# Kernel optimization log

Measured on AMD Instinct MI355X. Metric: run time of the kernel, lower is better.

The kernel has to match this reference:

```python
import jax, jax.numpy as jnp
import numpy as np
import math

D_MODEL = 1024
N_HEADS = 16
D_K = D_MODEL // N_HEADS
B, S = 4, 2048


def setup_inputs() -> dict:
    key = jax.random.key(0)
    ks = jax.random.split(key, 11)
    std = 1.0 / math.sqrt(D_MODEL)
    inp = {
        "query": jax.random.normal(ks[0], (B, S, D_MODEL), dtype=jnp.float32),
        "key_in": jax.random.normal(ks[1], (B, S, D_MODEL), dtype=jnp.float32),
        "value": jax.random.normal(ks[2], (B, S, D_MODEL), dtype=jnp.float32),
        "Wq": jax.random.normal(ks[3], (D_MODEL, D_MODEL), dtype=jnp.float32) * std,
        "bq": jnp.zeros((D_MODEL,), dtype=jnp.float32),
        "Wk": jax.random.normal(ks[4], (D_MODEL, D_MODEL), dtype=jnp.float32) * std,
        "bk": jnp.zeros((D_MODEL,), dtype=jnp.float32),
        "Wv": jax.random.normal(ks[5], (D_MODEL, D_MODEL), dtype=jnp.float32) * std,
        "bv": jnp.zeros((D_MODEL,), dtype=jnp.float32),
        "Wo": jax.random.normal(ks[6], (D_MODEL, D_MODEL), dtype=jnp.float32) * std,
        "bo": jnp.zeros((D_MODEL,), dtype=jnp.float32),
    }
    return inp


def reference(query, key_in, value, Wq, bq, Wk, bk, Wv, bv, Wo, bo):
    b, s, _ = query.shape
    scale = math.sqrt(D_K)
    # projections: nn.Linear computes x @ W.T + b
    Q = (query @ Wq.T + bq).reshape(b, s, N_HEADS, D_K).transpose(0, 2, 1, 3)
    K = (key_in @ Wk.T + bk).reshape(b, s, N_HEADS, D_K).transpose(0, 2, 1, 3)
    V = (value @ Wv.T + bv).reshape(b, s, N_HEADS, D_K).transpose(0, 2, 1, 3)
    # [b, h, s, s]
    scores = jnp.einsum("bhqd,bhkd->bhqk", Q, K) / scale
    causal = jnp.tril(jnp.ones((s, s), dtype=bool))
    scores = jnp.where(causal[None, None, :, :], scores, jnp.float32(-1e9))
    attn = jax.nn.softmax(scores, axis=-1)
    out = jnp.einsum("bhqk,bhkd->bhqd", attn, V)
    out = out.transpose(0, 2, 1, 3).reshape(b, s, D_MODEL)
    return out @ Wo.T + bo
```

## Files before the change

kernel.cpp:

```cpp
#include <hip/hip_runtime.h>
#include <hip/hip_bf16.h>
#include <cstdint>

#define DM   1024
#define NH   16
#define DKK  64
#define BB   4
#define SS   2048

typedef __attribute__((ext_vector_type(8)))  short short8;
typedef __attribute__((ext_vector_type(4)))  float f32x4;
typedef __attribute__((ext_vector_type(16))) float f32x16;

__device__ __forceinline__ unsigned short f2bf(float f) {
    union { float f; uint32_t u; } v; v.f = f;
    uint32_t u = v.u;
    uint32_t r = (u + 0x7FFFu + ((u >> 16) & 1u)) >> 16;
    return (unsigned short)r;
}

#define GLL(src, dst) __builtin_amdgcn_global_load_lds(                      \
        (__attribute__((address_space(1))) void*)(src),                      \
        (__attribute__((address_space(3))) void*)(dst), 16, 0, 0)

__global__ void cvt_w(const float* __restrict__ wq, const float* __restrict__ wk,
                      const float* __restrict__ wv, const float* __restrict__ wo,
                      unsigned short* __restrict__ dst)
{
    int i = blockIdx.x * 256 + threadIdx.x;
    int a = i >> 17;
    int r = i & 131071;
    int j = r >> 7, kb = r & 127;
    int kbs = (kb & ~7) | ((kb ^ j) & 7);
    const float* s = (a == 0 ? wq : a == 1 ? wk : a == 2 ? wv : wo) + (size_t)j * 1024 + kbs * 8;
    float4 f0 = *(const float4*)(s);
    float4 f1 = *(const float4*)(s + 4);
    union { uint32_t u[4]; short8 s8; } c;
    asm("v_cvt_pk_bf16_f32 %0, %1, %2" : "=v"(c.u[0]) : "v"(f0.x), "v"(f0.y));
    asm("v_cvt_pk_bf16_f32 %0, %1, %2" : "=v"(c.u[1]) : "v"(f0.z), "v"(f0.w));
    asm("v_cvt_pk_bf16_f32 %0, %1, %2" : "=v"(c.u[2]) : "v"(f1.x), "v"(f1.y));
    asm("v_cvt_pk_bf16_f32 %0, %1, %2" : "=v"(c.u[3]) : "v"(f1.z), "v"(f1.w));
    *(short8*)(dst + ((size_t)a << 20) + (size_t)j * 1024 + kb * 8) = c.s8;
}

__global__ __launch_bounds__(256) void gemm_qkv(
        const float* __restrict__ Aq, const float* __restrict__ Ak, const float* __restrict__ Av,
        const unsigned short* __restrict__ Wq, const unsigned short* __restrict__ Wk,
        const unsigned short* __restrict__ Wv,
        const float* __restrict__ bq, const float* __restrict__ bk, const float* __restrict__ bv,
        unsigned short* __restrict__ Qo, unsigned short* __restrict__ Ko,
        unsigned short* __restrict__ Vo, const float qscale)
{
    const int orig = blockIdx.z * 512 + blockIdx.y * 8 + blockIdx.x;
    const int wid  = (orig & 7) * 192 + (orig >> 3);
    const int z    = wid >> 9;
    const int rem  = wid & 511;
    const int brow = (rem >> 3) * 128;
    const int bcol = (rem & 7) * 128;

    const float* A           = (z == 0) ? Aq : (z == 1) ? Ak : Av;
    const unsigned short* Bw = (z == 0) ? Wq : (z == 1) ? Wk : Wv;
    const float* bias        = (z == 0) ? bq : (z == 1) ? bk : bv;

    __shared__ __align__(16) unsigned short lA[128 * 64];
    __shared__ __align__(16) unsigned short lB[2][128 * 64];

    const int tid = threadIdx.x;
    const int w = tid >> 6, l = tid & 63;
    const int wr = (w >> 1) * 64, wc = (w & 1) * 64;
    const int lrow = l & 15;
    const int hi = l >> 4;
    const int sr = l >> 3, scb = l & 7;

    const float* aga[4];
    int awb[4];
#pragma unroll
    for (int i = 0; i < 4; ++i) {
        const int chunk = w * 4 + i;
        const int r = chunk * 8 + sr;
        aga[i] = A + (size_t)(brow + r) * 1024 + scb * 8;
        awb[i] = chunk * 1024 + sr * 128 + ((scb ^ sr) << 4);
    }

    f32x4 areg[4][2];
    f32x4 acc[4][4] = {};

#pragma unroll
    for (int i = 0; i < 4; ++i) {
        const int chunk = w * 4 + i;
        const int r = chunk * 8 + sr;
        GLL(Bw + (size_t)(bcol + r) * 1024 + scb * 8, lB[0] + chunk * 512);
    }
#pragma unroll
    for (int i = 0; i < 4; ++i) {
        areg[i][0] = *(const f32x4*)(aga[i]);
        areg[i][1] = *(const f32x4*)(aga[i] + 4);
    }

    for (int t = 0; t < 16; ++t) {
#pragma unroll
        for (int i = 0; i < 4; ++i) {
            union { uint32_t u[4]; short8 s8; } c;
            asm("v_cvt_pk_bf16_f32 %0, %1, %2" : "=v"(c.u[0]) : "v"(areg[i][0][0]), "v"(areg[i][0][1]));
            asm("v_cvt_pk_bf16_f32 %0, %1, %2" : "=v"(c.u[1]) : "v"(areg[i][0][2]), "v"(areg[i][0][3]));
            asm("v_cvt_pk_bf16_f32 %0, %1, %2" : "=v"(c.u[2]) : "v"(areg[i][1][0]), "v"(areg[i][1][1]));
            asm("v_cvt_pk_bf16_f32 %0, %1, %2" : "=v"(c.u[3]) : "v"(areg[i][1][2]), "v"(areg[i][1][3]));
            *(short8*)((char*)lA + awb[i]) = c.s8;
        }
        if (t < 15) {
            const int k0n = (t + 1) * 64;
#pragma unroll
            for (int i = 0; i < 4; ++i) {
                areg[i][0] = *(const f32x4*)(aga[i] + k0n);
                areg[i][1] = *(const f32x4*)(aga[i] + k0n + 4);
            }
#pragma unroll
            for (int i = 0; i < 4; ++i) {
                const int chunk = w * 4 + i;
                const int r = chunk * 8 + sr;
                GLL(Bw + (size_t)(bcol + r) * 1024 + k0n + scb * 8, lB[(t + 1) & 1] + chunk * 512);
            }
            asm volatile("s_waitcnt vmcnt(12) lgkmcnt(0)" ::: "memory");
        } else {
            asm volatile("s_waitcnt vmcnt(0) lgkmcnt(0)" ::: "memory");
        }
        __builtin_amdgcn_s_barrier();
        const unsigned short* lb = lB[t & 1];
        __builtin_amdgcn_s_setprio(1);
#pragma unroll
        for (int kk = 0; kk < 2; ++kk) {
            short8 af[4], bf[4];
#pragma unroll
            for (int m = 0; m < 4; ++m) {
                const int row = wr + m * 16 + lrow;
                const int pb = (kk * 4 + hi) ^ (row & 7);
                af[m] = *(const short8*)((const char*)lA + row * 128 + (pb << 4));
            }
#pragma unroll
            for (int n = 0; n < 4; ++n) {
                const int row = wc + n * 16 + lrow;
                const int pb = (kk * 4 + hi) ^ (row & 7);
                bf[n] = *(const short8*)((const char*)lb + row * 128 + (pb << 4));
            }
#pragma unroll
            for (int m = 0; m < 4; ++m)
#pragma unroll
                for (int n = 0; n < 4; ++n)
                    acc[m][n] = __builtin_amdgcn_mfma_f32_16x16x32_bf16(af[m], bf[n], acc[m][n], 0, 0, 0);
        }
        __builtin_amdgcn_s_setprio(0);
        asm volatile("" ::: "memory");
        __builtin_amdgcn_s_barrier();
        asm volatile("" ::: "memory");
    }

    const float ascale = (z == 0) ? qscale : 1.0f;
#pragma unroll
    for (int m = 0; m < 4; ++m) {
#pragma unroll
        for (int n = 0; n < 4; ++n) {
            const int i0 = brow + wr + m * 16 + (l >> 4) * 4;
            const int j  = bcol + wc + n * 16 + lrow;
            const float bj = bias[j];
            const int hh = j >> 6, d = j & 63;
            if (z < 2) {
                unsigned short* Cb = (z == 0) ? Qo : Ko;
#pragma unroll
                for (int t = 0; t < 4; ++t) {
                    const int i = i0 + t;
                    const int b = i >> 11, s = i & 2047;
                    Cb[(((size_t)(b * NH + hh) * SS) + s) * DKK + d] = f2bf((acc[m][n][t] + bj) * ascale);
                }
            } else {
                const int b = i0 >> 11, s0 = i0 & 2047;
                ushort4 pk;
                pk.x = f2bf(acc[m][n][0] + bj);
                pk.y = f2bf(acc[m][n][1] + bj);
                pk.z = f2bf(acc[m][n][2] + bj);
                pk.w = f2bf(acc[m][n][3] + bj);
                *(ushort4*)(Vo + (((size_t)(b * NH + hh) * DKK) + d) * SS + s0) = pk;
            }
        }
    }
}

__global__ void gemm_out(const unsigned short* __restrict__ A,
                         const unsigned short* __restrict__ Bw,
                         const float* __restrict__ bias,
                         float* __restrict__ Cout)
{
    const int orig = blockIdx.y * 8 + blockIdx.x;
    const int wid  = (orig & 7) * 64 + (orig >> 3);
    const int brow = (wid >> 3) * 128;
    const int bcol = (wid & 7) * 128;

    __shared__ unsigned short lA[128 * 64];
    __shared__ unsigned short lB[128 * 64];
    const int tid = threadIdx.x;
    const int w = tid >> 6, l = tid & 63;
    const int wr = (w >> 1) * 64, wc = (w & 1) * 64;
    const int lrow = l & 15;
    const int hi = l >> 4;
    const int lk = hi * 8;
    const int sr = l >> 3;
    const int sc = (l & 7) * 8;
    f32x4 acc[4][4] = {};

    for (int k0 = 0; k0 < 1024; k0 += 64) {
#pragma unroll
        for (int i = 0; i < 4; ++i) {
            const int chunk = w * 4 + i;
            const int r = chunk * 8 + sr;
            GLL(A  + (size_t)(brow + r) * 1024 + k0 + sc, lA + chunk * 512);
            GLL(Bw + (size_t)(bcol + r) * 1024 + k0 + sc, lB + chunk * 512);
        }
        asm volatile("s_waitcnt vmcnt(0)" ::: "memory");
        __syncthreads();
#pragma unroll
        for (int kk = 0; kk < 2; ++kk) {
            short8 af[4], bfr[4];
#pragma unroll
            for (int m = 0; m < 4; ++m)
                af[m] = *(const short8*)(lA + (wr + m * 16 + lrow) * 64 + kk * 32 + lk);
#pragma unroll
            for (int n = 0; n < 4; ++n) {
                const int row = wc + n * 16 + lrow;
                const int pb = (kk * 4 + hi) ^ (row & 7);
                bfr[n] = *(const short8*)((const char*)lB + row * 128 + (pb << 4));
            }
#pragma unroll
            for (int m = 0; m < 4; ++m)
#pragma unroll
                for (int n = 0; n < 4; ++n)
                    acc[m][n] = __builtin_amdgcn_mfma_f32_16x16x32_bf16(af[m], bfr[n], acc[m][n], 0, 0, 0);
        }
        __syncthreads();
    }

#pragma unroll
    for (int m = 0; m < 4; ++m) {
#pragma unroll
        for (int n = 0; n < 4; ++n) {
            const int i0 = brow + wr + m * 16 + (l >> 4) * 4;
            const int j  = bcol + wc + n * 16 + lrow;
            const float bj = bias[j];
#pragma unroll
            for (int t = 0; t < 4; ++t)
                Cout[(size_t)(i0 + t) * DM + j] = acc[m][n][t] + bj;
        }
    }
}

__global__ __launch_bounds__(256) void attn_kernel(
        const unsigned short* __restrict__ Q,
        const unsigned short* __restrict__ K,
        const unsigned short* __restrict__ Vt,
        unsigned short* __restrict__ AO)
{
    const int flat = blockIdx.y * 16 + blockIdx.x;
    const int r8 = flat & 7, k8 = flat >> 3;
    const int bh = r8 * 8 + (k8 & 7);
    const int qchunk = 15 - (k8 >> 3);
    const int tid = threadIdx.x;
    const int w = tid >> 6, l = tid & 63;
    const int ln = l & 31, h = l >> 5;
    const int qb = qchunk * 128;
    const int q0w = qb + w * 32;

    __shared__ __align__(16) char lK[2][4096];
    __shared__ __align__(16) char lV[2][4096];

    const unsigned short* Qp = Q  + ((size_t)bh * SS + q0w) * DKK;
    const unsigned short* Kp = K  + (size_t)bh * SS * DKK;
    const unsigned short* Vp = Vt + (size_t)bh * DKK * SS;

    const int srow = tid >> 3, scb = tid & 7;
    const int swb = srow * 128 + ((scb * 16) ^ ((srow & 7) << 4));
    const unsigned short* ksrc = Kp + srow * DKK + scb * 8;
    const int vd = (scb < 4) ? srow : (srow + 32);
    const unsigned short* vsrc = Vp + (size_t)vd * SS + (scb & 3) * 8;

    int ka[4], va[4];
#pragma unroll
    for (int ks = 0; ks < 4; ++ks)
        ka[ks] = ln * 128 + ((ks * 32 + h * 16) ^ ((ln & 7) << 4));
#pragma unroll
    for (int c = 0; c < 4; ++c)
        va[c] = ln * 128 + ((c * 32 + h * 16) ^ ((ln & 7) << 4));

    short8 qf[4];
#pragma unroll
    for (int ks = 0; ks < 4; ++ks)
        qf[ks] = *(const short8*)(Qp + (size_t)ln * DKK + ks * 16 + h * 8);

    f32x16 o0 = {}, o1 = {};
    float lsum = 0.f;

    const int Tc = qb / 32;
    const int NT = Tc + 4;

    auto compute = [&](int t, int buf) {
        const char* kb = lK[buf];
        const char* vb = lV[buf];
        short8 kf[4];
#pragma unroll
        for (int ks = 0; ks < 4; ++ks) kf[ks] = *(const short8*)(kb + ka[ks]);

        f32x16 s = {};
        __builtin_amdgcn_s_setprio(1);
#pragma unroll
        for (int ks = 0; ks < 4; ++ks)
            s = __builtin_amdgcn_mfma_f32_32x32x16_bf16(kf[ks], qf[ks], s, 0, 0, 0);
        __builtin_amdgcn_s_setprio(0);

        const bool diag = (t == Tc + w);
#pragma unroll
        for (int r = 0; r < 16; ++r) {
            float e;
            asm("v_exp_f32 %0, %1" : "=v"(e) : "v"(s[r]));
            if (diag) {
                const int crow = (r & 3) + 8 * (r >> 2) + 4 * h;
                e = (crow > ln) ? 0.f : e;
            }
            s[r] = e;
            lsum += e;
        }

        uint32_t pk[8];
#pragma unroll
        for (int i = 0; i < 8; ++i) {
            uint32_t d;
            asm("v_cvt_pk_bf16_f32 %0, %1, %2" : "=v"(d) : "v"(s[2 * i]), "v"(s[2 * i + 1]));
            pk[i] = d;
        }
        asm("v_permlane32_swap_b32 %0, %1" : "+v"(pk[0]), "+v"(pk[2]));
        asm("v_permlane32_swap_b32 %0, %1" : "+v"(pk[1]), "+v"(pk[3]));
        asm("v_permlane32_swap_b32 %0, %1" : "+v"(pk[4]), "+v"(pk[6]));
        asm("v_permlane32_swap_b32 %0, %1" : "+v"(pk[5]), "+v"(pk[7]));

        union Ux { uint32_t u[4]; short8 s8; } pa0, pa1;
        pa0.u[0] = pk[0]; pa0.u[1] = pk[1]; pa0.u[2] = pk[2]; pa0.u[3] = pk[3];
        pa1.u[0] = pk[4]; pa1.u[1] = pk[5]; pa1.u[2] = pk[6]; pa1.u[3] = pk[7];

        short8 vf00 = *(const short8*)(vb + va[0]);
        short8 vf10 = *(const short8*)(vb + va[1]);
        short8 vf01 = *(const short8*)(vb + va[2]);
        short8 vf11 = *(const short8*)(vb + va[3]);

        __builtin_amdgcn_s_setprio(1);
        o0 = __builtin_amdgcn_mfma_f32_32x32x16_bf16(pa0.s8, vf00, o0, 0, 0, 0);
        o0 = __builtin_amdgcn_mfma_f32_32x32x16_bf16(pa1.s8, vf10, o0, 0, 0, 0);
        o1 = __builtin_amdgcn_mfma_f32_32x32x16_bf16(pa0.s8, vf01, o1, 0, 0, 0);
        o1 = __builtin_amdgcn_mfma_f32_32x32x16_bf16(pa1.s8, vf11, o1, 0, 0, 0);
        __builtin_amdgcn_s_setprio(0);
    };

    short8 kA = *(const short8*)(ksrc);
    short8 vA = *(const short8*)(vsrc);
    *(short8*)(&lK[0][swb]) = kA;
    *(short8*)(&lV[0][swb]) = vA;
    kA = *(const short8*)(ksrc + 2048);
    vA = *(const short8*)(vsrc + 32);
    short8 kB = {}, vB = {};
    __syncthreads();

    int t = 0, buf = 0;
    for (;;) {
        if (t + 2 < NT) {
            kB = *(const short8*)(ksrc + (size_t)(t + 2) * 2048);
            vB = *(const short8*)(vsrc + (size_t)(t + 2) * 32);
        }
        if (t <= Tc + w) compute(t, buf);
        if (t + 1 < NT) {
            *(short8*)(&lK[buf ^ 1][swb]) = kA;
            *(short8*)(&lV[buf ^ 1][swb]) = vA;
        }
        __syncthreads();
        buf ^= 1;
        if (++t == NT) break;

        if (t + 2 < NT) {
            kA = *(const short8*)(ksrc + (size_t)(t + 2) * 2048);
            vA = *(const short8*)(vsrc + (size_t)(t + 2) * 32);
        }
        if (t <= Tc + w) compute(t, buf);
        if (t + 1 < NT) {
            *(short8*)(&lK[buf ^ 1][swb]) = kB;
            *(short8*)(&lV[buf ^ 1][swb]) = vB;
        }
        __syncthreads();
        buf ^= 1;
        if (++t == NT) break;
    }

    lsum += __shfl_xor(lsum, 32, 64);
    const float rcp = 1.0f / lsum;

    const int bb = bh >> 4, hh = bh & 15;
#pragma unroll
    for (int r = 0; r < 16; ++r) {
        const int crow = (r & 3) + 8 * (r >> 2) + 4 * h;
        const float rl = __shfl(rcp, crow, 64);
        const size_t row = (size_t)(bb * SS + q0w + crow) * DM + hh * DKK;
        AO[row + ln]      = f2bf(o0[r] * rl);
        AO[row + 32 + ln] = f2bf(o1[r] * rl);
    }
}

extern "C" void kernel_launch(void* const* d_in, const int* in_sizes, int n_in,
                              void* d_out, int out_size, void* d_ws, size_t ws_size,
                              hipStream_t stream)
{
    const float* query  = (const float*)d_in[0];
    const float* key_in = (const float*)d_in[1];
    const float* value  = (const float*)d_in[2];
    const float* Wq = (const float*)d_in[3];
    const float* bq = (const float*)d_in[4];
    const float* Wk = (const float*)d_in[5];
    const float* bk = (const float*)d_in[6];
    const float* Wv = (const float*)d_in[7];
    const float* bv = (const float*)d_in[8];
    const float* Wo = (const float*)d_in[9];
    const float* bo = (const float*)d_in[10];

    const size_t NACT = (size_t)BB * SS * DM;
    const size_t NWT  = (size_t)DM * DM;

    unsigned short* ws  = (unsigned short*)d_ws;
    unsigned short* wqb = ws;
    unsigned short* wkb = wqb + NWT;
    unsigned short* wvb = wkb + NWT;
    unsigned short* wob = wvb + NWT;
    unsigned short* Qb  = wob + NWT;
    unsigned short* Kb  = Qb + NACT;
    unsigned short* Vtb = Kb + NACT;
    unsigned short* AOb = Vtb + NACT;

    cvt_w<<<2048, 256, 0, stream>>>(Wq, Wk, Wv, Wo, ws);

    const float QSCALE = 0.125f * 1.44269504088896f;
    dim3 gq(DM / 128, (BB * SS) / 128, 3);
    gemm_qkv<<<gq, 256, 0, stream>>>(query, key_in, value, wqb, wkb, wvb,
                                     bq, bk, bv, Qb, Kb, Vtb, QSCALE);

    attn_kernel<<<dim3(16, 64), 256, 0, stream>>>(Qb, Kb, Vtb, AOb);

    dim3 gg(DM / 128, (BB * SS) / 128);
    gemm_out<<<gg, 256, 0, stream>>>(AOb, wob, bo, (float*)d_out);
}
```

Measured before the change: 166.6 us.

## Deepen A-operand prefetch in QKV GEMM and software-pipeline output GEMM

The QKV projection now keeps two register sets of fp32 A tiles in flight (aX/aY), prefetching two K-steps ahead while B tiles are double-buffered in LDS via direct global-to-LDS loads. The output projection GEMM, which previously loaded A and B synchronously each step with a full vmcnt(0) wait, gets the same structure: A goes through registers with two-deep prefetch into a swizzled LDS layout, and B is double-buffered. This is meant to hide global memory latency behind MFMA work. The cost is more registers, which may reduce occupancy, and hand-tuned waitcnt values that must match the exact number of loads in flight.

```diff
diff --git a/kernel.cpp b/kernel.cpp
--- a/kernel.cpp
+++ b/kernel.cpp
@@ -73,86 +73,109 @@
     const int sr = l >> 3, scb = l & 7;
 
     const float* aga[4];
-    int awb[4];
+    const unsigned short* bga[4];
+    int awb[4], lbo[4];
 #pragma unroll
     for (int i = 0; i < 4; ++i) {
         const int chunk = w * 4 + i;
         const int r = chunk * 8 + sr;
         aga[i] = A + (size_t)(brow + r) * 1024 + scb * 8;
+        bga[i] = Bw + (size_t)(bcol + r) * 1024 + scb * 8;
         awb[i] = chunk * 1024 + sr * 128 + ((scb ^ sr) << 4);
-    }
-
-    f32x4 areg[4][2];
+        lbo[i] = chunk * 512;
+    }
+
+    f32x4 aX[4][2], aY[4][2];
     f32x4 acc[4][4] = {};
 
 #pragma unroll
-    for (int i = 0; i < 4; ++i) {
-        const int chunk = w * 4 + i;
-        const int r = chunk * 8 + sr;
-        GLL(Bw + (size_t)(bcol + r) * 1024 + scb * 8, lB[0] + chunk * 512);
-    }
-#pragma unroll
-    for (int i = 0; i < 4; ++i) {
-        areg[i][0] = *(const f32x4*)(aga[i]);
-        areg[i][1] = *(const f32x4*)(aga[i] + 4);
-    }
-
-    for (int t = 0; t < 16; ++t) {
-#pragma unroll
-        for (int i = 0; i < 4; ++i) {
-            union { uint32_t u[4]; short8 s8; } c;
-            asm("v_cvt_pk_bf16_f32 %0, %1, %2" : "=v"(c.u[0]) : "v"(areg[i][0][0]), "v"(areg[i][0][1]));
-            asm("v_cvt_pk_bf16_f32 %0, %1, %2" : "=v"(c.u[1]) : "v"(areg[i][0][2]), "v"(areg[i][0][3]));
-            asm("v_cvt_pk_bf16_f32 %0, %1, %2" : "=v"(c.u[2]) : "v"(areg[i][1][0]), "v"(areg[i][1][1]));
-            asm("v_cvt_pk_bf16_f32 %0, %1, %2" : "=v"(c.u[3]) : "v"(areg[i][1][2]), "v"(areg[i][1][3]));
-            *(short8*)((char*)lA + awb[i]) = c.s8;
-        }
-        if (t < 15) {
-            const int k0n = (t + 1) * 64;
-#pragma unroll
-            for (int i = 0; i < 4; ++i) {
-                areg[i][0] = *(const f32x4*)(aga[i] + k0n);
-                areg[i][1] = *(const f32x4*)(aga[i] + k0n + 4);
-            }
-#pragma unroll
-            for (int i = 0; i < 4; ++i) {
-                const int chunk = w * 4 + i;
-                const int r = chunk * 8 + sr;
-                GLL(Bw + (size_t)(bcol + r) * 1024 + k0n + scb * 8, lB[(t + 1) & 1] + chunk * 512);
-            }
-            asm volatile("s_waitcnt vmcnt(12) lgkmcnt(0)" ::: "memory");
-        } else {
-            asm volatile("s_waitcnt vmcnt(0) lgkmcnt(0)" ::: "memory");
-        }
-        __builtin_amdgcn_s_barrier();
-        const unsigned short* lb = lB[t & 1];
-        __builtin_amdgcn_s_setprio(1);
-#pragma unroll
-        for (int kk = 0; kk < 2; ++kk) {
-            short8 af[4], bf[4];
-#pragma unroll
-            for (int m = 0; m < 4; ++m) {
-                const int row = wr + m * 16 + lrow;
-                const int pb = (kk * 4 + hi) ^ (row & 7);
-                af[m] = *(const short8*)((const char*)lA + row * 128 + (pb << 4));
-            }
-#pragma unroll
-            for (int n = 0; n < 4; ++n) {
-                const int row = wc + n * 16 + lrow;
-                const int pb = (kk * 4 + hi) ^ (row & 7);
-                bf[n] = *(const short8*)((const char*)lb + row * 128 + (pb << 4));
-            }
-#pragma unroll
-            for (int m = 0; m < 4; ++m)
-#pragma unroll
-                for (int n = 0; n < 4; ++n)
-                    acc[m][n] = __builtin_amdgcn_mfma_f32_16x16x32_bf16(af[m], bf[n], acc[m][n], 0, 0, 0);
-        }
-        __builtin_amdgcn_s_setprio(0);
+    for (int i = 0; i < 4; ++i) GLL(bga[i], lB[0] + lbo[i]);
+#pragma unroll
+    for (int i = 0; i < 4; ++i) { aX[i][0] = *(const f32x4*)(aga[i]); aX[i][1] = *(const f32x4*)(aga[i] + 4); }
+#pragma unroll
+    for (int i = 0; i < 4; ++i) { aY[i][0] = *(const f32x4*)(aga[i] + 64); aY[i][1] = *(const f32x4*)(aga[i] + 64 + 4); }
+
+#define QKV_CVT(CUR)                                                                              \
+    _Pragma("unroll")                                                                             \
+    for (int i = 0; i < 4; ++i) {                                                                 \
+        union { uint32_t u[4]; short8 s8; } c;                                                    \
+        asm("v_cvt_pk_bf16_f32 %0, %1, %2" : "=v"(c.u[0]) : "v"(CUR[i][0][0]), "v"(CUR[i][0][1]));\
+        asm("v_cvt_pk_bf16_f32 %0, %1, %2" : "=v"(c.u[1]) : "v"(CUR[i][0][2]), "v"(CUR[i][0][3]));\
+        asm("v_cvt_pk_bf16_f32 %0, %1, %2" : "=v"(c.u[2]) : "v"(CUR[i][1][0]), "v"(CUR[i][1][1]));\
+        asm("v_cvt_pk_bf16_f32 %0, %1, %2" : "=v"(c.u[3]) : "v"(CUR[i][1][2]), "v"(CUR[i][1][3]));\
+        *(short8*)((char*)lA + awb[i]) = c.s8;                                                    \
+    }
+
+#define QKV_MFMA(LB)                                                                              \
+    {                                                                                             \
+        const unsigned short* lb = (LB);                                                          \
+        __builtin_amdgcn_s_setprio(1);                                                            \
+        _Pragma("unroll")                                                                         \
+        for (int kk = 0; kk < 2; ++kk) {                                                          \
+            short8 af[4], bf[4];                                                                  \
+            _Pragma("unroll")                                                                     \
+            for (int m = 0; m < 4; ++m) {                                                         \
+                const int row = wr + m * 16 + lrow;                                               \
+                const int pb = (kk * 4 + hi) ^ (row & 7);                                         \
+                af[m] = *(const short8*)((const char*)lA + row * 128 + (pb << 4));                \
+            }                                                                                     \
+            _Pragma("unroll")                                                                     \
+            for (int n = 0; n < 4; ++n) {                                                         \
+                const int row = wc + n * 16 + lrow;                                               \
+                const int pb = (kk * 4 + hi) ^ (row & 7);                                         \
+                bf[n] = *(const short8*)((const char*)lb + row * 128 + (pb << 4));                \
+            }                                                                                     \
+            _Pragma("unroll")                                                                     \
+            for (int m = 0; m < 4; ++m)                                                           \
+                _Pragma("unroll")                                                                 \
+                for (int n = 0; n < 4; ++n)                                                       \
+                    acc[m][n] = __builtin_amdgcn_mfma_f32_16x16x32_bf16(af[m], bf[n], acc[m][n], 0, 0, 0); \
+        }                                                                                         \
+        __builtin_amdgcn_s_setprio(0);                                                            \
+    }
+
+    for (int t = 0; t < 14; t += 2) {
+        QKV_CVT(aX);
+        {
+            const int ko = (t + 2) * 64;
+#pragma unroll
+            for (int i = 0; i < 4; ++i) { aX[i][0] = *(const f32x4*)(aga[i] + ko); aX[i][1] = *(const f32x4*)(aga[i] + ko + 4); }
+            const int kb = (t + 1) * 64;
+#pragma unroll
+            for (int i = 0; i < 4; ++i) GLL(bga[i] + kb, lB[1] + lbo[i]);
+        }
+        asm volatile("s_waitcnt vmcnt(12) lgkmcnt(0)" ::: "memory");
+        __builtin_amdgcn_s_barrier();
+        QKV_MFMA(lB[0]);
         asm volatile("" ::: "memory");
         __builtin_amdgcn_s_barrier();
+        QKV_CVT(aY);
+        {
+            const int ko = (t + 3) * 64;
+#pragma unroll
+            for (int i = 0; i < 4; ++i) { aY[i][0] = *(const f32x4*)(aga[i] + ko); aY[i][1] = *(const f32x4*)(aga[i] + ko + 4); }
+            const int kb = (t + 2) * 64;
+#pragma unroll
+            for (int i = 0; i < 4; ++i) GLL(bga[i] + kb, lB[0] + lbo[i]);
+        }
+        asm volatile("s_waitcnt vmcnt(12) lgkmcnt(0)" ::: "memory");
+        __builtin_amdgcn_s_barrier();
+        QKV_MFMA(lB[1]);
         asm volatile("" ::: "memory");
-    }
+        __builtin_amdgcn_s_barrier();
+    }
+    QKV_CVT(aX);
+#pragma unroll
+    for (int i = 0; i < 4; ++i) GLL(bga[i] + 15 * 64, lB[1] + lbo[i]);
+    asm volatile("s_waitcnt vmcnt(4) lgkmcnt(0)" ::: "memory");
+    __builtin_amdgcn_s_barrier();
+    QKV_MFMA(lB[0]);
+    asm volatile("" ::: "memory");
+    __builtin_amdgcn_s_barrier();
+    QKV_CVT(aY);
+    asm volatile("s_waitcnt vmcnt(0) lgkmcnt(0)" ::: "memory");
+    __builtin_amdgcn_s_barrier();
+    QKV_MFMA(lB[1]);
 
     const float ascale = (z == 0) ? qscale : 1.0f;
 #pragma unroll
@@ -182,60 +205,130 @@
             }
         }
     }
+#undef QKV_CVT
+#undef QKV_MFMA
 }
 
-__global__ void gemm_out(const unsigned short* __restrict__ A,
-                         const unsigned short* __restrict__ Bw,
-                         const float* __restrict__ bias,
-                         float* __restrict__ Cout)
+__global__ __launch_bounds__(256) void gemm_out(
+        const unsigned short* __restrict__ A,
+        const unsigned short* __restrict__ Bw,
+        const float* __restrict__ bias,
+        float* __restrict__ Cout)
 {
     const int orig = blockIdx.y * 8 + blockIdx.x;
     const int wid  = (orig & 7) * 64 + (orig >> 3);
     const int brow = (wid >> 3) * 128;
     const int bcol = (wid & 7) * 128;
 
-    __shared__ unsigned short lA[128 * 64];
-    __shared__ unsigned short lB[128 * 64];
+    __shared__ __align__(16) unsigned short lA[128 * 64];
+    __shared__ __align__(16) unsigned short lB[2][128 * 64];
+
     const int tid = threadIdx.x;
     const int w = tid >> 6, l = tid & 63;
     const int wr = (w >> 1) * 64, wc = (w & 1) * 64;
     const int lrow = l & 15;
     const int hi = l >> 4;
-    const int lk = hi * 8;
-    const int sr = l >> 3;
-    const int sc = (l & 7) * 8;
+    const int sr = l >> 3, scb = l & 7;
+
+    const unsigned short* aga[4];
+    const unsigned short* bga[4];
+    int awb[4], lbo[4];
+#pragma unroll
+    for (int i = 0; i < 4; ++i) {
+        const int chunk = w * 4 + i;
+        const int r = chunk * 8 + sr;
+        aga[i] = A  + (size_t)(brow + r) * 1024 + scb * 8;
+        bga[i] = Bw + (size_t)(bcol + r) * 1024 + scb * 8;
+        awb[i] = chunk * 1024 + sr * 128 + ((scb ^ sr) << 4);
+        lbo[i] = chunk * 512;
+    }
+
+    short8 aX[4], aY[4];
     f32x4 acc[4][4] = {};
 
-    for (int k0 = 0; k0 < 1024; k0 += 64) {
-#pragma unroll
-        for (int i = 0; i < 4; ++i) {
-            const int chunk = w * 4 + i;
-            const int r = chunk * 8 + sr;
-            GLL(A  + (size_t)(brow + r) * 1024 + k0 + sc, lA + chunk * 512);
-            GLL(Bw + (size_t)(bcol + r) * 1024 + k0 + sc, lB + chunk * 512);
-        }
-        asm volatile("s_waitcnt vmcnt(0)" ::: "memory");
-        __syncthreads();
-#pragma unroll
-        for (int kk = 0; kk < 2; ++kk) {
-            short8 af[4], bfr[4];
-#pragma unroll
-            for (int m = 0; m < 4; ++m)
-                af[m] = *(const short8*)(lA + (wr + m * 16 + lrow) * 64 + kk * 32 + lk);
-#pragma unroll
-            for (int n = 0; n < 4; ++n) {
-                const int row = wc + n * 16 + lrow;
-                const int pb = (kk * 4 + hi) ^ (row & 7);
-                bfr[n] = *(const short8*)((const char*)lB + row * 128 + (pb << 4));
-            }
-#pragma unroll
-            for (int m = 0; m < 4; ++m)
-#pragma unroll
-                for (int n = 0; n < 4; ++n)
-                    acc[m][n] = __builtin_amdgcn_mfma_f32_16x16x32_bf16(af[m], bfr[n], acc[m][n], 0, 0, 0);
-        }
-        __syncthreads();
-    }
+#pragma unroll
+    for (int i = 0; i < 4; ++i) GLL(bga[i], lB[0] + lbo[i]);
+#pragma unroll
+    for (int i = 0; i < 4; ++i) aX[i] = *(const short8*)(aga[i]);
+#pragma unroll
+    for (int i = 0; i < 4; ++i) aY[i] = *(const short8*)(aga[i] + 64);
+
+#define OUT_WR(CUR)                                                     \
+    _Pragma("unroll")                                                   \
+    for (int i = 0; i < 4; ++i)                                         \
+        *(short8*)((char*)lA + awb[i]) = CUR[i];
+
+#define OUT_MFMA(LB)                                                                              \
+    {                                                                                             \
+        const unsigned short* lb = (LB);                                                          \
+        __builtin_amdgcn_s_setprio(1);                                                            \
+        _Pragma("unroll")                                                                         \
+        for (int kk = 0; kk < 2; ++kk) {                                                          \
+            short8 af[4], bf[4];                                                                  \
+            _Pragma("unroll")                                                                     \
+            for (int m = 0; m < 4; ++m) {                                                         \
+                const int row = wr + m * 16 + lrow;                                               \
+                const int pb = (kk * 4 + hi) ^ (row & 7);                                         \
+                af[m] = *(const short8*)((const char*)lA + row * 128 + (pb << 4));                \
+            }                                                                                     \
+            _Pragma("unroll")                                                                     \
+            for (int n = 0; n < 4; ++n) {                                                         \
+                const int row = wc + n * 16 + lrow;                                               \
+                const int pb = (kk * 4 + hi) ^ (row & 7);                                         \
+                bf[n] = *(const short8*)((const char*)lb + row * 128 + (pb << 4));                \
+            }                                                                                     \
+            _Pragma("unroll")                                                                     \
+            for (int m = 0; m < 4; ++m)                                                           \
+                _Pragma("unroll")                                                                 \
+                for (int n = 0; n < 4; ++n)                                                       \
+                    acc[m][n] = __builtin_amdgcn_mfma_f32_16x16x32_bf16(af[m], bf[n], acc[m][n], 0, 0, 0); \
+        }                                                                                         \
+        __builtin_amdgcn_s_setprio(0);                                                            \
+    }
+
+    for (int t = 0; t < 14; t += 2) {
+        OUT_WR(aX);
+        {
+            const int ko = (t + 2) * 64;
+#pragma unroll
+            for (int i = 0; i < 4; ++i) aX[i] = *(const short8*)(aga[i] + ko);
+            const int kb = (t + 1) * 64;
+#pragma unroll
+            for (int i = 0; i < 4; ++i) GLL(bga[i] + kb, lB[1] + lbo[i]);
+        }
+        asm volatile("s_waitcnt vmcnt(8) lgkmcnt(0)" ::: "memory");
+        __builtin_amdgcn_s_barrier();
+        OUT_MFMA(lB[0]);
+        asm volatile("" ::: "memory");
+        __builtin_amdgcn_s_barrier();
+
+        OUT_WR(aY);
+        {
+            const int ko = (t + 3) * 64;
+#pragma unroll
+            for (int i = 0; i < 4; ++i) aY[i] = *(const short8*)(aga[i] + ko);
+            const int kb = (t + 2) * 64;
+#pragma unroll
+            for (int i = 0; i < 4; ++i) GLL(bga[i] + kb, lB[0] + lbo[i]);
+        }
+        asm volatile("s_waitcnt vmcnt(8) lgkmcnt(0)" ::: "memory");
+        __builtin_amdgcn_s_barrier();
+        OUT_MFMA(lB[1]);
+        asm volatile("" ::: "memory");
+        __builtin_amdgcn_s_barrier();
+    }
+    OUT_WR(aX);
+#pragma unroll
+    for (int i = 0; i < 4; ++i) GLL(bga[i] + 15 * 64, lB[1] + lbo[i]);
+    asm volatile("s_waitcnt vmcnt(4) lgkmcnt(0)" ::: "memory");
+    __builtin_amdgcn_s_barrier();
+    OUT_MFMA(lB[0]);
+    asm volatile("" ::: "memory");
+    __builtin_amdgcn_s_barrier();
+    OUT_WR(aY);
+    asm volatile("s_waitcnt vmcnt(0) lgkmcnt(0)" ::: "memory");
+    __builtin_amdgcn_s_barrier();
+    OUT_MFMA(lB[1]);
 
 #pragma unroll
     for (int m = 0; m < 4; ++m) {
@@ -249,6 +342,8 @@
                 Cout[(size_t)(i0 + t) * DM + j] = acc[m][n][t] + bj;
         }
     }
+#undef OUT_WR
+#undef OUT_MFMA
 }
 
 __global__ __launch_bounds__(256) void attn_kernel(
```

After: 162.5 us. 2.5% less time.
